# Optimization experiments

Measured on AMD Instinct MI355X. Metric: run time of the kernel, lower is better.

## Reference

```python
import jax, jax.numpy as jnp
import numpy as np

B, L, E, H = 4, 4096, 1024, 16
D = E // H  # head_dim = 64
EPS = 1e-4


def setup_inputs() -> dict:
    key = jax.random.key(0)
    k1, k2, k3 = jax.random.split(key, 3)
    x = jax.random.normal(k1, (B, L, E), dtype=jnp.float32)
    W_qkv = jax.random.normal(k2, (E, 3 * E), dtype=jnp.float32) * (1.0 / np.sqrt(E))
    b_qkv = jnp.zeros((3 * E,), dtype=jnp.float32)
    W_out = jax.random.normal(k3, (E, E), dtype=jnp.float32) * (1.0 / np.sqrt(E))
    b_out = jnp.zeros((E,), dtype=jnp.float32)
    return {"x": x, "W_qkv": W_qkv, "b_qkv": b_qkv, "W_out": W_out, "b_out": b_out}


def reference(x, W_qkv, b_qkv, W_out, b_out):
    Bb, Ll, Ee = x.shape
    qkv = x @ W_qkv + b_qkv                      # [B, L, 3E]
    q, k, v = jnp.split(qkv, 3, axis=-1)
    # [B, H, L, D]
    q = q.reshape(Bb, Ll, H, D).transpose(0, 2, 1, 3)
    k = k.reshape(Bb, Ll, H, D).transpose(0, 2, 1, 3)
    v = v.reshape(Bb, Ll, H, D).transpose(0, 2, 1, 3)

    positions = jnp.arange(Ll, dtype=jnp.float32).reshape(1, 1, Ll, 1)
    cos_w = jnp.cos(jnp.pi / 2 * positions / Ll)
    sin_w = jnp.sin(jnp.pi / 2 * positions / Ll)

    q_prime = jax.nn.relu(q)
    k_prime = jax.nn.relu(k)

    q_cos, q_sin = q_prime * cos_w, q_prime * sin_w
    k_cos, k_sin = k_prime * cos_w, k_prime * sin_w

    # O(L) linear attention: accumulate KV outer products per head
    kv_cos = jnp.einsum('bhld,bhle->bhde', k_cos, v)      # [B,H,D,D]
    kv_sin = jnp.einsum('bhld,bhle->bhde', k_sin, v)
    context = (jnp.einsum('bhld,bhde->bhle', q_cos, kv_cos)
               + jnp.einsum('bhld,bhde->bhle', q_sin, kv_sin))  # [B,H,L,D]

    k_cos_sum = k_cos.sum(axis=2)                          # [B,H,D]
    k_sin_sum = k_sin.sum(axis=2)
    norm = (jnp.einsum('bhld,bhd->bhl', q_cos, k_cos_sum)
            + jnp.einsum('bhld,bhd->bhl', q_sin, k_sin_sum))

    output = context / (norm[..., None] + EPS)
    output = output.transpose(0, 2, 1, 3).reshape(Bb, Ll, Ee)
    return output @ W_out + b_out
```

## Files before the change

### kernel.cpp

```cpp
#include <hip/hip_runtime.h>
#include <hip/hip_bf16.h>
#include <cstdint>
#include <cstddef>

#define BB 4
#define LL 4096
#define HH 16
#define M1 16384
#define E3 3072
#define EE 1024
#define ANGC 3.8349519697141029e-4f
#define EPSC 1e-4f

typedef __attribute__((ext_vector_type(8))) short bf16x8;
typedef __attribute__((ext_vector_type(4))) float f32x4;
typedef __attribute__((ext_vector_type(8))) unsigned short us8;

static __device__ __forceinline__ float bf2f(unsigned short u) {
  union { unsigned int i; float f; } a; a.i = ((unsigned int)u) << 16; return a.f;
}
static __device__ __forceinline__ unsigned short f2bf(float x) {
  union { float f; unsigned int i; } a; a.f = x;
  unsigned int r = a.i + 0x7FFFu + ((a.i >> 16) & 1u);
  return (unsigned short)(r >> 16);
}
static __device__ __forceinline__ void gload16(const void* g, void* l) {
  __builtin_amdgcn_global_load_lds((const __attribute__((address_space(1))) void*)g,
                                   (__attribute__((address_space(3))) void*)l, 16, 0, 0);
}

#define BAR()   asm volatile("s_barrier" ::: "memory")
#define VMC4()  asm volatile("s_waitcnt vmcnt(4)" ::: "memory")
#define VMC0()  asm volatile("s_waitcnt vmcnt(0)" ::: "memory")
#define PRIO1() __builtin_amdgcn_s_setprio(1)
#define PRIO0() __builtin_amdgcn_s_setprio(0)

static __device__ __forceinline__ void transpose_body(const float* __restrict__ src,
                                                      unsigned short* __restrict__ dst,
                                                      int R, int C, int bx, int by,
                                                      float (*tile)[33]) {
  int c0 = bx * 32, r0 = by * 32;
  int tx = threadIdx.x & 31, ty = threadIdx.x >> 5;
#pragma unroll
  for (int k = 0; k < 4; ++k)
    tile[ty + 8*k][tx] = src[(size_t)(r0 + ty + 8*k) * C + c0 + tx];
  __syncthreads();
#pragma unroll
  for (int k = 0; k < 4; ++k)
    dst[(size_t)(c0 + ty + 8*k) * R + r0 + tx] = f2bf(tile[tx][ty + 8*k]);
}

__global__ __launch_bounds__(256) void k_prep(const float* __restrict__ x,
                                              const float* __restrict__ Wq,
                                              const float* __restrict__ Wo,
                                              unsigned short* __restrict__ xb,
                                              unsigned short* __restrict__ WqT,
                                              unsigned short* __restrict__ WoT,
                                              float* __restrict__ zbase) {
  __shared__ float tile[32][33];
  const int bid = blockIdx.x;
  if (bid < 8192) {
    int i = bid * 256 + threadIdx.x;
    const float4* s = (const float4*)x + (size_t)i * 2;
    float4 a = s[0], b = s[1];
    us8 o;
    o[0]=f2bf(a.x); o[1]=f2bf(a.y); o[2]=f2bf(a.z); o[3]=f2bf(a.w);
    o[4]=f2bf(b.x); o[5]=f2bf(b.y); o[6]=f2bf(b.z); o[7]=f2bf(b.w);
    *(us8*)(xb + (size_t)i * 8) = o;
  } else if (bid < 8192 + 3072) {
    int r = bid - 8192;
    transpose_body(Wq, WqT, 1024, 3072, r % 96, r / 96, tile);
  } else if (bid < 11264 + 1024) {
    int r = bid - 11264;
    transpose_body(Wo, WoT, 1024, 1024, r % 32, r / 32, tile);
  } else {
    int r = bid - 12288;
    float4 z = {0.f, 0.f, 0.f, 0.f};
    *(float4*)((char*)zbase + (size_t)r * 4096 + threadIdx.x * 16) = z;
  }
}


static __device__ __forceinline__ bf16x8 rdfrag(const char* base, int row, int ck) {
  return *(const bf16x8*)(base + row * 128 + (((ck) ^ ((row) & 7)) << 4));
}

static __device__ __forceinline__ void stage2h(const unsigned short* __restrict__ base,
                                               size_t off, size_t rowK64, char* ldst) {
  gload16(base + off, ldst);
  gload16(base + off + rowK64, ldst + 8192);
}

#define PH_FIRST(AbP, BbP, AR)                                                  \
  do {                                                                          \
    _Pragma("unroll")                                                           \
    for (int n = 0; n < 4; ++n) {                                               \
      const int br = wc * 64 + n * 16 + lr;                                     \
      bF[n][0] = rdfrag((BbP), br, lg);                                         \
      bF[n][1] = rdfrag((BbP), br, 4 + lg);                                     \
    }                                                                           \
    AR[0][0] = rdfrag((AbP), wr * 128 + lr, lg);                                \
    AR[0][1] = rdfrag((AbP), wr * 128 + lr, 4 + lg);                            \
    AR[1][0] = rdfrag((AbP), wr * 128 + 16 + lr, lg);                           \
    AR[1][1] = rdfrag((AbP), wr * 128 + 16 + lr, 4 + lg);                       \
  } while (0)

#define PH_A(AbP, mb, AR)                                                       \
  do {                                                                          \
    AR[0][0] = rdfrag((AbP), wr * 128 + (mb) * 16 + lr, lg);                    \
    AR[0][1] = rdfrag((AbP), wr * 128 + (mb) * 16 + lr, 4 + lg);                \
    AR[1][0] = rdfrag((AbP), wr * 128 + (mb) * 16 + 16 + lr, lg);               \
    AR[1][1] = rdfrag((AbP), wr * 128 + (mb) * 16 + 16 + lr, 4 + lg);           \
  } while (0)

#define MMA16(mb, AR)                                                           \
  do {                                                                          \
    _Pragma("unroll")                                                           \
    for (int kk = 0; kk < 2; ++kk) {                                            \
      _Pragma("unroll")                                                         \
      for (int n = 0; n < 4; ++n) {                                             \
        acc[(mb)][n] = __builtin_amdgcn_mfma_f32_16x16x32_bf16(                 \
            AR[0][kk], bF[n][kk], acc[(mb)][n], 0, 0, 0);                       \
        acc[(mb) + 1][n] = __builtin_amdgcn_mfma_f32_16x16x32_bf16(             \
            AR[1][kk], bF[n][kk], acc[(mb) + 1][n], 0, 0, 0);                   \
      }                                                                         \
    }                                                                           \
  } while (0)

template<int MODE>
__global__ __launch_bounds__(512, 2) void k_gemm256(const unsigned short* __restrict__ A,
                                                    const unsigned short* __restrict__ Bt,
                                                    const float* __restrict__ bias,
                                                    void* __restrict__ Cout,
                                                    int N, int K) {
  __shared__ __align__(16) unsigned short lds[4][16384];
  const int tid = threadIdx.x;
  const int wid = tid >> 6, lane = tid & 63;
  const int lr = lane & 15, lg = lane >> 4;
  const int wr = wid >> 2, wc = wid & 3;

  const int nx = gridDim.x;
  const int rawbid = blockIdx.y * nx + blockIdx.x;
  const int xcd = rawbid & 7, s = rawbid >> 3;
  const int g = s >> 5, r = s & 31;
  const int bm = (xcd * 8 + (r & 7)) * 256;
  const int bn = (g * 4 + (r >> 3)) * 256;

  char* LA0 = (char*)&lds[0][0];
  char* LB0 = (char*)&lds[1][0];
  char* LA1 = (char*)&lds[2][0];
  char* LB1 = (char*)&lds[3][0];

  f32x4 acc[8][4] = {};
  bf16x8 bF[4][2], aF[2][2], aG[2][2];

  const int rr = tid >> 3, cc = tid & 7;
  const size_t rowK64 = (size_t)64 * K, rowK128 = (size_t)128 * K;
  const size_t aoff = (size_t)(bm + rr) * K + ((cc ^ (rr & 7)) << 3);
  const size_t boff = (size_t)(bn + rr) * K + ((cc ^ (rr & 7)) << 3);

#define STAGE_A(h, kt, L) stage2h(A,  aoff + (h) * rowK128 + (kt), rowK64, (L) + (h) * 16384 + tid * 16)
#define STAGE_B(h, kt, L) stage2h(Bt, boff + (h) * rowK128 + (kt), rowK64, (L) + (h) * 16384 + tid * 16)

  const int NT = K >> 6, NI = NT >> 1;

  STAGE_A(0, 0, LA0); STAGE_A(1, 0, LA0);
  STAGE_B(0, 0, LB0); STAGE_B(1, 0, LB0);
  STAGE_B(0, 64, LB1); STAGE_B(1, 64, LB1);
  VMC4();
  BAR();

  for (int it = 0; it < NI; ++it) {
    const int kt1 = (2*it + 1) << 6;
    const int kt2 = (2*it + 2) << 6;
    const int kt3 = (2*it + 3) << 6;
    const bool s2 = kt2 < K, s3 = kt3 < K;

    PH_FIRST(LA0, LB0, aF);
    STAGE_A(0, kt1, LA1);
    PH_A(LA0, 2, aG);
    STAGE_A(1, kt1, LA1);
    PRIO1(); MMA16(0, aF); MMA16(2, aG); PRIO0();
    BAR();

    PH_A(LA0, 4, aF);
    if (s2) STAGE_B(0, kt2, LB0);
    PH_A(LA0, 6, aG);
    if (s2) STAGE_B(1, kt2, LB0);
    PRIO1(); MMA16(4, aF); MMA16(6, aG); PRIO0();
    if (it == NI - 1) { VMC0(); } else { VMC4(); }
    BAR();

    PH_FIRST(LA1, LB1, aF);
    if (s2) STAGE_A(0, kt2, LA0);
    PH_A(LA1, 2, aG);
    if (s2) STAGE_A(1, kt2, LA0);
    PRIO1(); MMA16(0, aF); MMA16(2, aG); PRIO0();
    BAR();

    PH_A(LA1, 4, aF);
    if (s3) STAGE_B(0, kt3, LB1);
    PH_A(LA1, 6, aG);
    if (s3) STAGE_B(1, kt3, LB1);
    PRIO1(); MMA16(4, aF); MMA16(6, aG); PRIO0();
    VMC4();
    BAR();
  }
#undef STAGE_A
#undef STAGE_B

  {
    float* strip = (float*)((char*)&lds[0][0] + wid * 16384);
    float bias_v[4]; bool relu_v[4];
#pragma unroll
    for (int n = 0; n < 4; ++n) {
      int col = bn + wc*64 + n*16 + lr;
      bias_v[n] = bias[col];
      relu_v[n] = (MODE == 0) && (col < 2048);
    }
#pragma unroll
    for (int m = 0; m < 8; ++m) {
#pragma unroll
      for (int n = 0; n < 4; ++n)
#pragma unroll
        for (int j = 0; j < 4; ++j) {
          float v = acc[m][n][j] + bias_v[n];
          if (relu_v[n]) v = fmaxf(v, 0.0f);
          strip[(lg*4 + j)*68 + n*16 + lr] = v;
        }
#pragma unroll
      for (int itr = 0; itr < 4; ++itr) {
        int ch = itr*64 + lane;
        int row = ch >> 4, cg = ch & 15;
        float4 v = *(const float4*)(strip + row*68 + cg*4);
        size_t base = (size_t)(bm + wr*128 + m*16 + row) * N + bn + wc*64 + cg*4;
        if (MODE == 0) {
          ushort4 o;
          o.x = f2bf(v.x); o.y = f2bf(v.y); o.z = f2bf(v.z); o.w = f2bf(v.w);
          *(ushort4*)((unsigned short*)Cout + base) = o;
        } else {
          *(float4*)((float*)Cout + base) = v;
        }
      }
    }
  }
}

static __device__ __forceinline__ int swz2(int d) { return (d & 7) ^ (d >> 3); }

__global__ __launch_bounds__(256) void k_stage2(const unsigned short* __restrict__ qkv,
                                                float* __restrict__ kvb,
                                                float* __restrict__ ksumb) {
  __shared__ __align__(16) unsigned short kcT[4096];
  __shared__ __align__(16) unsigned short ksT[4096];
  __shared__ __align__(16) unsigned short vT [4096];
  const int tid = threadIdx.x;
  const int head = blockIdx.y;
  const int b = head >> 4, h = head & 15;
  const int lane = tid & 63, wid = tid >> 6;
  const int lr = lane & 15, lg = lane >> 4;
  const int mt = wid >> 1, eh = wid & 1;
  const int pr = tid >> 3;
  const int pc = tid & 7;

  f32x4 acc[2][4] = {};
  float ksacc = 0.0f;
  const int mtk = tid >> 6, dk = tid & 63;
  const size_t qbase = (size_t)b * LL * E3;

  for (int sc = 0; sc < 16; ++sc) {
    const int lbase = blockIdx.x * 1024 + sc * 64;
    __syncthreads();
    {
      const int l0 = 2 * pr;
      const int p0 = lbase + l0;
      float s0, c0, s1, c1;
      __sincosf((float)p0 * ANGC, &s0, &c0);
      __sincosf((float)(p0 + 1) * ANGC, &s1, &c1);
      const unsigned short* kp = qkv + qbase + (size_t)p0 * E3 + 1024 + h*64 + pc*8;
      us8 kr0 = *(const us8*)kp;
      us8 kr1 = *(const us8*)(kp + E3);
      us8 vr0 = *(const us8*)(kp + 1024);
      us8 vr1 = *(const us8*)(kp + 1024 + E3);
      const int cch = pr >> 2, wb = (pr & 3) * 4;
#pragma unroll
      for (int i = 0; i < 8; ++i) {
        int d = pc*8 + i;
        float ka = bf2f(kr0[i]), kb = bf2f(kr1[i]);
        unsigned int kcp = (unsigned int)f2bf(c0*ka) | ((unsigned int)f2bf(c1*kb) << 16);
        unsigned int ksp = (unsigned int)f2bf(s0*ka) | ((unsigned int)f2bf(s1*kb) << 16);
        unsigned int vp  = (unsigned int)vr0[i] | ((unsigned int)vr1[i] << 16);
        int off = d*128 + ((cch ^ swz2(d)) << 4) + wb;
        *(unsigned int*)((char*)kcT + off) = kcp;
        *(unsigned int*)((char*)ksT + off) = ksp;
        *(unsigned int*)((char*)vT  + off) = vp;
      }
    }
    __syncthreads();
    if (tid < 128) {
      const unsigned short* basep = mtk ? ksT : kcT;
      float sum = 0.0f;
#pragma unroll
      for (int cch2 = 0; cch2 < 8; ++cch2) {
        us8 r2 = *(const us8*)((const char*)basep + dk*128 + ((cch2 ^ swz2(dk)) << 4));
#pragma unroll
        for (int i = 0; i < 8; ++i) sum += bf2f(r2[i]);
      }
      ksacc += sum;
    }
    {
      const unsigned short* kT = mt ? ksT : kcT;
      bf16x8 af[2][2], bf[2][4];
#pragma unroll
      for (int kk = 0; kk < 2; ++kk) {
#pragma unroll
        for (int m = 0; m < 2; ++m) {
          int e = eh*32 + m*16 + lr;
          af[kk][m] = *(const bf16x8*)((const char*)vT + e*128 + ((((kk*4)+lg) ^ swz2(e)) << 4));
        }
#pragma unroll
        for (int n = 0; n < 4; ++n) {
          int d = n*16 + lr;
          bf[kk][n] = *(const bf16x8*)((const char*)kT + d*128 + ((((kk*4)+lg) ^ swz2(d)) << 4));
        }
      }
#pragma unroll
      for (int kk = 0; kk < 2; ++kk)
#pragma unroll
        for (int m = 0; m < 2; ++m)
#pragma unroll
          for (int n = 0; n < 4; ++n)
            acc[m][n] = __builtin_amdgcn_mfma_f32_16x16x32_bf16(af[kk][m], bf[kk][n], acc[m][n], 0, 0, 0);
    }
  }
  float* dst = kvb + (size_t)head * 8192 + mt * 4096;
#pragma unroll
  for (int m = 0; m < 2; ++m)
#pragma unroll
    for (int n = 0; n < 4; ++n)
#pragma unroll
      for (int j = 0; j < 4; ++j) {
        int e = eh*32 + m*16 + lg*4 + j;
        int d = n*16 + lr;
        atomicAdd(&dst[e*64 + d], acc[m][n][j]);
      }
  if (tid < 128) atomicAdd(&ksumb[head*128 + mtk*64 + dk], ksacc);
}

__global__ __launch_bounds__(256) void k_stage3(const unsigned short* __restrict__ qkv,
                                                const float* __restrict__ kvb,
                                                const float* __restrict__ ksumb,
                                                unsigned short* __restrict__ att) {
  __shared__ __align__(16) unsigned short Bl[144 * 64];
  const int tid = threadIdx.x;
  const int head = blockIdx.y;
  const int b = head >> 4, h = head & 15;
  const int l0 = blockIdx.x * 128;
  const int lane = tid & 63, w = tid >> 6;
  const int lr = lane & 15, lg = lane >> 4;

  {
    int c = tid >> 1, half = tid & 1;
    const float* src = kvb + (size_t)head * 8192 + (c >> 6) * 4096 + (c & 63) * 64 + half * 32;
    float fv[32];
#pragma unroll
    for (int q = 0; q < 8; ++q) *(float4*)(fv + q*4) = *(const float4*)(src + q*4);
#pragma unroll
    for (int q2 = 0; q2 < 4; ++q2) {
      us8 o;
#pragma unroll
      for (int i = 0; i < 8; ++i) o[i] = f2bf(fv[q2*8 + i]);
      int chunk = half*4 + q2;
      *(us8*)((char*)Bl + c*128 + ((chunk ^ (c & 7)) << 4)) = o;
    }
    if (tid < 16) {
      int cc = 128 + (tid >> 3), q = tid & 7;
      const float* s2 = ksumb + head*128 + (tid >> 3)*64 + q*8;
      us8 o;
#pragma unroll
      for (int i = 0; i < 8; ++i) o[i] = f2bf(s2[i]);
      *(us8*)((char*)Bl + cc*128 + ((q ^ (cc & 7)) << 4)) = o;
    } else if (tid < 128) {
      int idx = tid - 16;
      int cc = 130 + (idx >> 3), q = idx & 7;
      us8 o = {0,0,0,0,0,0,0,0};
      *(us8*)((char*)Bl + cc*128 + ((q ^ (cc & 7)) << 4)) = o;
    }
  }
  __syncthreads();

  f32x4 acc[2][9] = {};
  bf16x8 af[2][2];
  const size_t qrow0 = (size_t)(b * LL + l0 + w * 32);
#pragma unroll
  for (int kk = 0; kk < 2; ++kk)
#pragma unroll
    for (int m = 0; m < 2; ++m)
      af[m][kk] = *(const bf16x8*)(qkv + (qrow0 + m*16 + lr) * E3 + h*64 + kk*32 + lg*8);
#pragma unroll
  for (int kk = 0; kk < 2; ++kk)
#pragma unroll
    for (int n = 0; n < 9; ++n) {
      int cc = n*16 + lr;
      bf16x8 bb = *(const bf16x8*)((const char*)Bl + cc*128 + ((((kk*4)+lg) ^ (cc & 7)) << 4));
#pragma unroll
      for (int m = 0; m < 2; ++m)
        acc[m][n] = __builtin_amdgcn_mfma_f32_16x16x32_bf16(af[m][kk], bb, acc[m][n], 0, 0, 0);
    }

  __syncthreads();
  unsigned short* strip = (unsigned short*)Bl + w * 2048;
#pragma unroll
  for (int m = 0; m < 2; ++m)
#pragma unroll
    for (int j = 0; j < 4; ++j) {
      int rloc = m*16 + lg*4 + j;
      int pos = l0 + w*32 + rloc;
      float s_, c_;
      __sincosf((float)pos * ANGC, &s_, &c_);
      float nc = __shfl(acc[m][8][j], lane & 48, 64);
      float ns = __shfl(acc[m][8][j], (lane & 48) | 1, 64);
      float rn = 1.0f / (c_ * nc + s_ * ns + EPSC);
#pragma unroll
      for (int n = 0; n < 4; ++n) {
        float ctx = (c_ * acc[m][n][j] + s_ * acc[m][n+4][j]) * rn;
        strip[rloc*64 + n*16 + lr] = f2bf(ctx);
      }
    }
  __syncthreads();
#pragma unroll
  for (int p = 0; p < 4; ++p) {
    int ch = p*64 + lane;
    int row = ch >> 3, piece = ch & 7;
    us8 o = *(const us8*)(strip + row*64 + piece*8);
    *(us8*)(att + (size_t)(b*LL + l0 + w*32 + row) * EE + h*64 + piece*8) = o;
  }
}

extern "C" void kernel_launch(void* const* d_in, const int* in_sizes, int n_in,
                              void* d_out, int out_size, void* d_ws, size_t ws_size,
                              hipStream_t stream) {
  const float* x     = (const float*)d_in[0];
  const float* W_qkv = (const float*)d_in[1];
  const float* b_qkv = (const float*)d_in[2];
  const float* W_out = (const float*)d_in[3];
  const float* b_out = (const float*)d_in[4];

  char* w = (char*)d_ws;
  unsigned short* xb  = (unsigned short*)(w);
  unsigned short* qkv = (unsigned short*)(w + 33554432);
  unsigned short* WqT = (unsigned short*)(w + 134217728);
  unsigned short* WoT = (unsigned short*)(w + 140509184);
  float* kvb   = (float*)(w + 142606336);
  float* ksum  = (float*)(w + 144703488);
  unsigned short* att = xb;

  k_prep<<<12808, 256, 0, stream>>>(x, W_qkv, W_out, xb, WqT, WoT, kvb);
  k_gemm256<0><<<dim3(12, 64), 512, 0, stream>>>(xb, WqT, b_qkv, (void*)qkv, 3072, 1024);
  k_stage2<<<dim3(4, 64), 256, 0, stream>>>(qkv, kvb, ksum);
  k_stage3<<<dim3(32, 64), 256, 0, stream>>>(qkv, kvb, ksum, att);
  k_gemm256<1><<<dim3(4, 64), 512, 0, stream>>>(att, WoT, b_out, d_out, 1024, 1024);
}
```

Before: 202.8 us.

## Use 16 waves per block in 256x256 GEMM, halving per-wave M tile

The GEMM block goes from 512 to 1024 threads (16 waves), and each wave now owns a 64x64 output sub-tile instead of 128x64. Accumulators drop from 8x4 to 4x4 fragments, and each thread issues one global-to-LDS load per stage instead of two, with the vmcnt waits adjusted to match. The pipeline phases are restructured, and the epilogue strip per wave shrinks so 16 waves fit in LDS. The aim is more waves to hide latency and lower register pressure. The cost is reduced per-wave data reuse, with more LDS fragment reads per MFMA and more barrier participants.

```diff
diff --git a/kernel.cpp b/kernel.cpp
--- a/kernel.cpp
+++ b/kernel.cpp
@@ -30,7 +30,7 @@
 }
 
 #define BAR()   asm volatile("s_barrier" ::: "memory")
-#define VMC4()  asm volatile("s_waitcnt vmcnt(4)" ::: "memory")
+#define VMC2()  asm volatile("s_waitcnt vmcnt(2)" ::: "memory")
 #define VMC0()  asm volatile("s_waitcnt vmcnt(0)" ::: "memory")
 #define PRIO1() __builtin_amdgcn_s_setprio(1)
 #define PRIO0() __builtin_amdgcn_s_setprio(0)
@@ -85,12 +85,6 @@
   return *(const bf16x8*)(base + row * 128 + (((ck) ^ ((row) & 7)) << 4));
 }
 
-static __device__ __forceinline__ void stage2h(const unsigned short* __restrict__ base,
-                                               size_t off, size_t rowK64, char* ldst) {
-  gload16(base + off, ldst);
-  gload16(base + off + rowK64, ldst + 8192);
-}
-
 #define PH_FIRST(AbP, BbP, AR)                                                  \
   do {                                                                          \
     _Pragma("unroll")                                                           \
@@ -99,18 +93,18 @@
       bF[n][0] = rdfrag((BbP), br, lg);                                         \
       bF[n][1] = rdfrag((BbP), br, 4 + lg);                                     \
     }                                                                           \
-    AR[0][0] = rdfrag((AbP), wr * 128 + lr, lg);                                \
-    AR[0][1] = rdfrag((AbP), wr * 128 + lr, 4 + lg);                            \
-    AR[1][0] = rdfrag((AbP), wr * 128 + 16 + lr, lg);                           \
-    AR[1][1] = rdfrag((AbP), wr * 128 + 16 + lr, 4 + lg);                       \
+    AR[0][0] = rdfrag((AbP), wr * 64 + lr, lg);                                 \
+    AR[0][1] = rdfrag((AbP), wr * 64 + lr, 4 + lg);                             \
+    AR[1][0] = rdfrag((AbP), wr * 64 + 16 + lr, lg);                            \
+    AR[1][1] = rdfrag((AbP), wr * 64 + 16 + lr, 4 + lg);                        \
   } while (0)
 
 #define PH_A(AbP, mb, AR)                                                       \
   do {                                                                          \
-    AR[0][0] = rdfrag((AbP), wr * 128 + (mb) * 16 + lr, lg);                    \
-    AR[0][1] = rdfrag((AbP), wr * 128 + (mb) * 16 + lr, 4 + lg);                \
-    AR[1][0] = rdfrag((AbP), wr * 128 + (mb) * 16 + 16 + lr, lg);               \
-    AR[1][1] = rdfrag((AbP), wr * 128 + (mb) * 16 + 16 + lr, 4 + lg);           \
+    AR[0][0] = rdfrag((AbP), wr * 64 + (mb) * 16 + lr, lg);                     \
+    AR[0][1] = rdfrag((AbP), wr * 64 + (mb) * 16 + lr, 4 + lg);                 \
+    AR[1][0] = rdfrag((AbP), wr * 64 + (mb) * 16 + 16 + lr, lg);                \
+    AR[1][1] = rdfrag((AbP), wr * 64 + (mb) * 16 + 16 + lr, 4 + lg);            \
   } while (0)
 
 #define MMA16(mb, AR)                                                           \
@@ -128,11 +122,11 @@
   } while (0)
 
 template<int MODE>
-__global__ __launch_bounds__(512, 2) void k_gemm256(const unsigned short* __restrict__ A,
-                                                    const unsigned short* __restrict__ Bt,
-                                                    const float* __restrict__ bias,
-                                                    void* __restrict__ Cout,
-                                                    int N, int K) {
+__global__ __launch_bounds__(1024) void k_gemm256(const unsigned short* __restrict__ A,
+                                                  const unsigned short* __restrict__ Bt,
+                                                  const float* __restrict__ bias,
+                                                  void* __restrict__ Cout,
+                                                  int N, int K) {
   __shared__ __align__(16) unsigned short lds[4][16384];
   const int tid = threadIdx.x;
   const int wid = tid >> 6, lane = tid & 63;
@@ -151,23 +145,23 @@
   char* LA1 = (char*)&lds[2][0];
   char* LB1 = (char*)&lds[3][0];
 
-  f32x4 acc[8][4] = {};
-  bf16x8 bF[4][2], aF[2][2], aG[2][2];
+  f32x4 acc[4][4] = {};
+  bf16x8 bF[4][2], aF[2][2];
 
   const int rr = tid >> 3, cc = tid & 7;
-  const size_t rowK64 = (size_t)64 * K, rowK128 = (size_t)128 * K;
+  const size_t rowK128 = (size_t)128 * K;
   const size_t aoff = (size_t)(bm + rr) * K + ((cc ^ (rr & 7)) << 3);
   const size_t boff = (size_t)(bn + rr) * K + ((cc ^ (rr & 7)) << 3);
 
-#define STAGE_A(h, kt, L) stage2h(A,  aoff + (h) * rowK128 + (kt), rowK64, (L) + (h) * 16384 + tid * 16)
-#define STAGE_B(h, kt, L) stage2h(Bt, boff + (h) * rowK128 + (kt), rowK64, (L) + (h) * 16384 + tid * 16)
+#define STAGE_A(h, kt, L) gload16(A  + aoff + (h) * rowK128 + (kt), (L) + (h) * 16384 + tid * 16)
+#define STAGE_B(h, kt, L) gload16(Bt + boff + (h) * rowK128 + (kt), (L) + (h) * 16384 + tid * 16)
 
   const int NT = K >> 6, NI = NT >> 1;
 
   STAGE_A(0, 0, LA0); STAGE_A(1, 0, LA0);
   STAGE_B(0, 0, LB0); STAGE_B(1, 0, LB0);
   STAGE_B(0, 64, LB1); STAGE_B(1, 64, LB1);
-  VMC4();
+  VMC2();
   BAR();
 
   for (int it = 0; it < NI; ++it) {
@@ -178,39 +172,32 @@
 
     PH_FIRST(LA0, LB0, aF);
     STAGE_A(0, kt1, LA1);
-    PH_A(LA0, 2, aG);
     STAGE_A(1, kt1, LA1);
-    PRIO1(); MMA16(0, aF); MMA16(2, aG); PRIO0();
     BAR();
-
-    PH_A(LA0, 4, aF);
-    if (s2) STAGE_B(0, kt2, LB0);
-    PH_A(LA0, 6, aG);
-    if (s2) STAGE_B(1, kt2, LB0);
-    PRIO1(); MMA16(4, aF); MMA16(6, aG); PRIO0();
-    if (it == NI - 1) { VMC0(); } else { VMC4(); }
+    PRIO1(); MMA16(0, aF); PRIO0();
+
+    PH_A(LA0, 2, aF);
+    if (s2) { STAGE_B(0, kt2, LB0); STAGE_B(1, kt2, LB0); }
+    PRIO1(); MMA16(2, aF); PRIO0();
+    if (it == NI - 1) { VMC0(); } else { VMC2(); }
     BAR();
 
     PH_FIRST(LA1, LB1, aF);
-    if (s2) STAGE_A(0, kt2, LA0);
-    PH_A(LA1, 2, aG);
-    if (s2) STAGE_A(1, kt2, LA0);
-    PRIO1(); MMA16(0, aF); MMA16(2, aG); PRIO0();
+    if (s2) { STAGE_A(0, kt2, LA0); STAGE_A(1, kt2, LA0); }
     BAR();
-
-    PH_A(LA1, 4, aF);
-    if (s3) STAGE_B(0, kt3, LB1);
-    PH_A(LA1, 6, aG);
-    if (s3) STAGE_B(1, kt3, LB1);
-    PRIO1(); MMA16(4, aF); MMA16(6, aG); PRIO0();
-    VMC4();
+    PRIO1(); MMA16(0, aF); PRIO0();
+
+    PH_A(LA1, 2, aF);
+    if (s3) { STAGE_B(0, kt3, LB1); STAGE_B(1, kt3, LB1); }
+    PRIO1(); MMA16(2, aF); PRIO0();
+    VMC2();
     BAR();
   }
 #undef STAGE_A
 #undef STAGE_B
 
   {
-    float* strip = (float*)((char*)&lds[0][0] + wid * 16384);
+    float* strip = (float*)((char*)&lds[0][0] + wid * 4352);
     float bias_v[4]; bool relu_v[4];
 #pragma unroll
     for (int n = 0; n < 4; ++n) {
@@ -219,7 +206,7 @@
       relu_v[n] = (MODE == 0) && (col < 2048);
     }
 #pragma unroll
-    for (int m = 0; m < 8; ++m) {
+    for (int m = 0; m < 4; ++m) {
 #pragma unroll
       for (int n = 0; n < 4; ++n)
 #pragma unroll
@@ -233,7 +220,7 @@
         int ch = itr*64 + lane;
         int row = ch >> 4, cg = ch & 15;
         float4 v = *(const float4*)(strip + row*68 + cg*4);
-        size_t base = (size_t)(bm + wr*128 + m*16 + row) * N + bn + wc*64 + cg*4;
+        size_t base = (size_t)(bm + wr*64 + m*16 + row) * N + bn + wc*64 + cg*4;
         if (MODE == 0) {
           ushort4 o;
           o.x = f2bf(v.x); o.y = f2bf(v.y); o.z = f2bf(v.z); o.w = f2bf(v.w);
@@ -456,8 +443,8 @@
   unsigned short* att = xb;
 
   k_prep<<<12808, 256, 0, stream>>>(x, W_qkv, W_out, xb, WqT, WoT, kvb);
-  k_gemm256<0><<<dim3(12, 64), 512, 0, stream>>>(xb, WqT, b_qkv, (void*)qkv, 3072, 1024);
+  k_gemm256<0><<<dim3(12, 64), 1024, 0, stream>>>(xb, WqT, b_qkv, (void*)qkv, 3072, 1024);
   k_stage2<<<dim3(4, 64), 256, 0, stream>>>(qkv, kvb, ksum);
   k_stage3<<<dim3(32, 64), 256, 0, stream>>>(qkv, kvb, ksum, att);
-  k_gemm256<1><<<dim3(4, 64), 512, 0, stream>>>(att, WoT, b_out, d_out, 1024, 1024);
-}
+  k_gemm256<1><<<dim3(4, 64), 1024, 0, stream>>>(att, WoT, b_out, d_out, 1024, 1024);
+}
```

Result: slower. 315.4 us (+55.5%).
